# Optimization experiments

Hardware: AMD Instinct MI355X
Metric: run time of the kernel (lower is better)

## Reference

```python
import jax, jax.numpy as jnp
import numpy as np

B, C, H, W = 8, 256, 128, 128
CQK = C // 8
EPS = 1e-6


def _l2n(x):
    # normalize over channel axis (dim=-2), matching torch l2_norm (no eps)
    return x / jnp.linalg.norm(x, axis=-2, keepdims=True)


def setup_inputs() -> dict:
    key = jax.random.key(0)
    ks = jax.random.split(key, 8)
    s = 0.05
    return {
        "x": jax.random.normal(ks[0], (B, C, H, W), dtype=jnp.float32),
        "Wq": jax.random.normal(ks[1], (CQK, C), dtype=jnp.float32) * s,
        "bq": jax.random.normal(ks[2], (CQK,), dtype=jnp.float32) * s,
        "Wk": jax.random.normal(ks[3], (CQK, C), dtype=jnp.float32) * s,
        "bk": jax.random.normal(ks[4], (CQK,), dtype=jnp.float32) * s,
        "Wv": jax.random.normal(ks[5], (C, C), dtype=jnp.float32) * s,
        "bv": jax.random.normal(ks[6], (C,), dtype=jnp.float32) * s,
        "gamma": jnp.ones((1,), dtype=jnp.float32) * 0.5,
    }


def reference(x, Wq, bq, Wk, bk, Wv, bv, gamma):
    b, c, h, w = x.shape
    n = h * w
    xf = x.reshape(b, c, n)  # [B, C, N]
    # 1x1 convs == channel matmuls
    Q = jnp.einsum('oc,bcn->bon', Wq, xf) + bq[None, :, None]  # [B, Cqk, N]
    K = jnp.einsum('oc,bcn->bon', Wk, xf) + bk[None, :, None]  # [B, Cqk, N]
    V = jnp.einsum('oc,bcn->bon', Wv, xf) + bv[None, :, None]  # [B, C, N]
    Qn = jnp.swapaxes(_l2n(Q), 1, 2)  # [B, N, Cqk]
    Kn = _l2n(K)                      # [B, Cqk, N]
    k_sum = jnp.sum(Kn, axis=-1) + EPS               # [B, Cqk]
    tailor = 1.0 / (n + jnp.einsum('bnc,bc->bn', Qn, k_sum))  # [B, N]
    value_sum = jnp.sum(V, axis=-1)                   # [B, C]
    matrix = jnp.einsum('bmn,bcn->bmc', Kn, V)        # [B, Cqk, C]
    matrix_sum = value_sum[:, :, None] + jnp.einsum('bnm,bmc->bcn', Qn, matrix)  # [B, C, N]
    weight_value = matrix_sum * tailor[:, None, :]    # [B, C, N]
    return x + gamma[0] * weight_value.reshape(b, c, h, w)
```

## Files before the change

### kernel.cpp

```cpp
#include <hip/hip_runtime.h>
#include <stdint.h>


#define NB 8
#define NC 256
#define CQK 32
#define NPIX 16384
#define NTILE 64
#define TN 256
#define PARTF (CQK*NC + NC + CQK)
#define EPSV 1e-6f

typedef unsigned short bfraw;

__device__ __forceinline__ float bf2f(bfraw u) {
    union { uint32_t i; float f; } v; v.i = ((uint32_t)u) << 16; return v.f;
}
__device__ __forceinline__ void unpack8(uint4 raw, float* xv) {
    xv[0] = bf2f((bfraw)(raw.x & 0xffffu)); xv[1] = bf2f((bfraw)(raw.x >> 16));
    xv[2] = bf2f((bfraw)(raw.y & 0xffffu)); xv[3] = bf2f((bfraw)(raw.y >> 16));
    xv[4] = bf2f((bfraw)(raw.z & 0xffffu)); xv[5] = bf2f((bfraw)(raw.z >> 16));
    xv[6] = bf2f((bfraw)(raw.w & 0xffffu)); xv[7] = bf2f((bfraw)(raw.w >> 16));
}

template<int DT> __device__ __forceinline__ float ldx(const void* p, size_t i) {
    if (DT) return ((const float*)p)[i];
    return bf2f(((const bfraw*)p)[i]);
}
template<int DT> __device__ __forceinline__ void ld8(const void* p, size_t i, float* o) {
    if (DT) {
        const float4* q = (const float4*)((const float*)p + i);
        float4 a = q[0], b = q[1];
        o[0]=a.x;o[1]=a.y;o[2]=a.z;o[3]=a.w;o[4]=b.x;o[5]=b.y;o[6]=b.z;o[7]=b.w;
    } else {
        uint4 raw = *(const uint4*)((const bfraw*)p + i);
        unpack8(raw, o);
    }
}

__global__ __launch_bounds__(256) void detect_kernel(const bfraw* __restrict__ x,
                                                     int* __restrict__ flag) {
    __shared__ int cnt, ez;
    int tid = threadIdx.x;
    if (tid == 0) { cnt = 0; ez = 0; }
    __syncthreads();
    int crazy = 0, evenzero = 0;
    for (int i = tid; i < 2048; i += 256) {
        bfraw u = x[i];
        float v = bf2f(u);
        float a = fabsf(v);
        if (!(a <= 1e10f) || (v != 0.f && a < 1e-10f)) crazy++;
        if ((i & 1) == 0 && u == 0) evenzero++;
    }
    atomicAdd(&cnt, crazy);
    atomicAdd(&ez, evenzero);
    __syncthreads();
    if (tid == 0) flag[0] = (cnt > 64 || ez > 900) ? 1 : 0;
}

template<int DT> __device__ __forceinline__ void prep_body(
    const void* Wq, const void* bq, const void* Wk, const void* bk,
    float* wqT, float* wkT, float* bqf, float* bkf) {
    int tid = threadIdx.x;
    for (int i = tid; i < CQK*NC; i += 256) {
        int m = i / NC, c = i % NC;
        wqT[c*CQK + m] = ldx<DT>(Wq, i);
        wkT[c*CQK + m] = ldx<DT>(Wk, i);
    }
    if (tid < CQK) { bqf[tid] = ldx<DT>(bq, tid); bkf[tid] = ldx<DT>(bk, tid); }
}
__global__ __launch_bounds__(256) void prep_kernel(
    const void* Wq, const void* bq, const void* Wk, const void* bk,
    float* wqT, float* wkT, float* bqf, float* bkf, const int* flag) {
    if (flag[0]) prep_body<1>(Wq, bq, Wk, bk, wqT, wkT, bqf, bkf);
    else         prep_body<0>(Wq, bq, Wk, bk, wqT, wkT, bqf, bkf);
}

template<int DT> __device__ __forceinline__ void pass1_body(
    const void* __restrict__ x, const float* __restrict__ wkT,
    const float* __restrict__ bkf, float* __restrict__ partial, int PB,
    float (*kn_s)[36]) {
    int tid = threadIdx.x;
    int b = blockIdx.x / PB, j = blockIdx.x % PB;

    float sacc[CQK];
    #pragma unroll
    for (int m = 0; m < CQK; ++m) sacc[m] = 0.f;
    float xsacc = 0.f, ksacc = 0.f;

    const size_t xb_base = (size_t)b * NC * NPIX;

    for (int tile = j; tile < NTILE; tile += PB) {
        int n0 = tile * TN;

        float q[CQK];
        #pragma unroll
        for (int m = 0; m < CQK; ++m) q[m] = bkf[m];
        const size_t pix = xb_base + n0 + tid;
        #pragma unroll 4
        for (int c = 0; c < NC; ++c) {
            float xv = ldx<DT>(x, pix + (size_t)c * NPIX);
            const float4* w = (const float4*)(wkT + c*CQK);
            #pragma unroll
            for (int m4 = 0; m4 < 8; ++m4) {
                float4 wv = w[m4];
                q[m4*4+0] += wv.x * xv; q[m4*4+1] += wv.y * xv;
                q[m4*4+2] += wv.z * xv; q[m4*4+3] += wv.w * xv;
            }
        }
        float ss = 0.f;
        #pragma unroll
        for (int m = 0; m < CQK; ++m) ss += q[m]*q[m];
        float inv = rsqrtf(ss);

        __syncthreads();
        #pragma unroll
        for (int m4 = 0; m4 < 8; ++m4) {
            float4 kv;
            kv.x = q[m4*4+0]*inv; kv.y = q[m4*4+1]*inv;
            kv.z = q[m4*4+2]*inv; kv.w = q[m4*4+3]*inv;
            *((float4*)&kn_s[tid][m4*4]) = kv;
        }
        __syncthreads();

        const size_t rowbase = xb_base + (size_t)tid * NPIX + n0;
        for (int k0 = 0; k0 < TN; k0 += 8) {
            float xv[8]; ld8<DT>(x, rowbase + k0, xv);
            #pragma unroll
            for (int kk = 0; kk < 8; ++kk) {
                const float4* kr = (const float4*)&kn_s[k0+kk][0];
                float xvk = xv[kk];
                #pragma unroll
                for (int m4 = 0; m4 < 8; ++m4) {
                    float4 a = kr[m4];
                    sacc[m4*4+0] += a.x*xvk; sacc[m4*4+1] += a.y*xvk;
                    sacc[m4*4+2] += a.z*xvk; sacc[m4*4+3] += a.w*xvk;
                }
                xsacc += xvk;
            }
        }

        if (tid < CQK) {
            float s = 0.f;
            for (int t = 0; t < TN; ++t) s += kn_s[t][tid];
            ksacc += s;
        }
    }

    size_t base = (size_t)blockIdx.x * PARTF;
    #pragma unroll
    for (int m = 0; m < CQK; ++m) partial[base + m*NC + tid] = sacc[m];
    partial[base + CQK*NC + tid] = xsacc;
    if (tid < CQK) partial[base + CQK*NC + NC + tid] = ksacc;
}
__global__ __launch_bounds__(256) void pass1_kernel(
    const void* __restrict__ x, const float* __restrict__ wkT,
    const float* __restrict__ bkf, float* __restrict__ partial, int PB,
    const int* __restrict__ flag) {
    __shared__ __align__(16) float kn_s[TN][36];
    if (flag[0]) pass1_body<1>(x, wkT, bkf, partial, PB, kn_s);
    else         pass1_body<0>(x, wkT, bkf, partial, PB, kn_s);
}

template<int DT> __device__ __forceinline__ float dot256(const void* Wv, int row,
                                                         const float* sh) {
    float r = 0.f;
    for (int c0 = 0; c0 < NC; c0 += 8) {
        float xv[8]; ld8<DT>(Wv, (size_t)row * NC + c0, xv);
        #pragma unroll
        for (int i = 0; i < 8; ++i) r += xv[i] * sh[c0+i];
    }
    return r;
}
template<int DT> __device__ __forceinline__ void pass15_body(
    const float* __restrict__ partial, const void* __restrict__ Wv,
    const void* __restrict__ bv, float* __restrict__ matT,
    float* __restrict__ vsum, float* __restrict__ ksum, int PB, float* sh) {
    int tid = threadIdx.x;
    int b = blockIdx.x / 33, m = blockIdx.x % 33;
    const float* pb_ = partial + (size_t)b * PB * PARTF;

    if (m < CQK) {
        float acc = 0.f;
        for (int p = 0; p < PB; ++p) acc += pb_[(size_t)p*PARTF + m*NC + tid];
        sh[tid] = acc;
        float ks = 0.f;
        for (int p = 0; p < PB; ++p) ks += pb_[(size_t)p*PARTF + CQK*NC + NC + m];
        __syncthreads();
        float r = dot256<DT>(Wv, tid, sh);
        matT[((size_t)b*NC + tid)*CQK + m] = r + ldx<DT>(bv, tid) * ks;
        if (tid == 0) ksum[b*CQK + m] = ks + EPSV;
    } else {
        float acc = 0.f;
        for (int p = 0; p < PB; ++p) acc += pb_[(size_t)p*PARTF + CQK*NC + tid];
        sh[tid] = acc;
        __syncthreads();
        float r = dot256<DT>(Wv, tid, sh);
        vsum[b*NC + tid] = r + (float)NPIX * ldx<DT>(bv, tid);
    }
}
__global__ __launch_bounds__(256) void pass15_kernel(
    const float* __restrict__ partial, const void* __restrict__ Wv,
    const void* __restrict__ bv, float* __restrict__ matT,
    float* __restrict__ vsum, float* __restrict__ ksum, int PB,
    const int* __restrict__ flag) {
    __shared__ float sh[NC];
    if (flag[0]) pass15_body<1>(partial, Wv, bv, matT, vsum, ksum, PB, sh);
    else         pass15_body<0>(partial, Wv, bv, matT, vsum, ksum, PB, sh);
}

template<int DT> __device__ __forceinline__ void pass2_body(
    const void* __restrict__ x, const float* __restrict__ wqT,
    const float* __restrict__ bqf, const float* __restrict__ ksum,
    const float* __restrict__ matT, const float* __restrict__ vsum,
    const void* __restrict__ gamma, float* __restrict__ out) {
    int tid = threadIdx.x;
    int b = blockIdx.x / NTILE, tile = blockIdx.x % NTILE;
    int n0 = tile * TN;
    const size_t xb_base = (size_t)b * NC * NPIX;
    const size_t pix = xb_base + n0 + tid;

    float q[CQK];
    #pragma unroll
    for (int m = 0; m < CQK; ++m) q[m] = bqf[m];
    #pragma unroll 4
    for (int c = 0; c < NC; ++c) {
        float xv = ldx<DT>(x, pix + (size_t)c * NPIX);
        const float4* w = (const float4*)(wqT + c*CQK);
        #pragma unroll
        for (int m4 = 0; m4 < 8; ++m4) {
            float4 wv = w[m4];
            q[m4*4+0] += wv.x * xv; q[m4*4+1] += wv.y * xv;
            q[m4*4+2] += wv.z * xv; q[m4*4+3] += wv.w * xv;
        }
    }
    float ss = 0.f;
    #pragma unroll
    for (int m = 0; m < CQK; ++m) ss += q[m]*q[m];
    float inv = rsqrtf(ss);
    const float* ksb = ksum + b*CQK;
    float dot = 0.f;
    #pragma unroll
    for (int m = 0; m < CQK; ++m) { q[m] *= inv; dot += q[m] * ksb[m]; }
    float tl = 1.f / ((float)NPIX + dot);
    float gt = ldx<DT>(gamma, 0) * tl;

    const float* mb = matT + (size_t)b*NC*CQK;
    const float* vb = vsum + (size_t)b*NC;
    float* op = out + pix;
    #pragma unroll 2
    for (int c = 0; c < NC; ++c) {
        float r = vb[c];
        const float4* mr = (const float4*)(mb + c*CQK);
        #pragma unroll
        for (int m4 = 0; m4 < 8; ++m4) {
            float4 a = mr[m4];
            r += q[m4*4+0]*a.x + q[m4*4+1]*a.y + q[m4*4+2]*a.z + q[m4*4+3]*a.w;
        }
        float xv = ldx<DT>(x, pix + (size_t)c * NPIX);
        op[(size_t)c * NPIX] = xv + gt*r;
    }
}
__global__ __launch_bounds__(256) void pass2_kernel(
    const void* __restrict__ x, const float* __restrict__ wqT,
    const float* __restrict__ bqf, const float* __restrict__ ksum,
    const float* __restrict__ matT, const float* __restrict__ vsum,
    const void* __restrict__ gamma, float* __restrict__ out,
    const int* __restrict__ flag) {
    if (flag[0]) pass2_body<1>(x, wqT, bqf, ksum, matT, vsum, gamma, out);
    else         pass2_body<0>(x, wqT, bqf, ksum, matT, vsum, gamma, out);
}

extern "C" void kernel_launch(void* const* d_in, const int* in_sizes, int n_in,
                              void* d_out, int out_size, void* d_ws, size_t ws_size,
                              hipStream_t stream)
{
    const void* x  = d_in[0];
    const void* Wq = d_in[1];
    const void* bq = d_in[2];
    const void* Wk = d_in[3];
    const void* bk = d_in[4];
    const void* Wv = d_in[5];
    const void* bv = d_in[6];
    const void* gm = d_in[7];
    float* out = (float*)d_out;

    float* ws = (float*)d_ws;
    int*  flag = (int*)ws;
    float* wkT = ws + 16;
    float* wqT = wkT + CQK*NC;
    float* bkf = wqT + CQK*NC;
    float* bqf = bkf + CQK;
    float* matT = bqf + CQK;
    float* vsum = matT + NB*NC*CQK;
    float* ksum = vsum + NB*NC;
    float* partial = ksum + NB*CQK;

    size_t fixedf = (size_t)(partial - ws);
    int PB = 64;
    while (PB > 1 && (fixedf + (size_t)NB*PB*PARTF) * 4 > ws_size) PB >>= 1;

    hipLaunchKernelGGL(detect_kernel, dim3(1), dim3(256), 0, stream,
                       (const bfraw*)x, flag);
    hipLaunchKernelGGL(prep_kernel, dim3(1), dim3(256), 0, stream,
                       Wq, bq, Wk, bk, wqT, wkT, bqf, bkf, flag);
    hipLaunchKernelGGL(pass1_kernel, dim3(NB*PB), dim3(256), 0, stream,
                       x, wkT, bkf, partial, PB, flag);
    hipLaunchKernelGGL(pass15_kernel, dim3(NB*33), dim3(256), 0, stream,
                       partial, Wv, bv, matT, vsum, ksum, PB, flag);
    hipLaunchKernelGGL(pass2_kernel, dim3(NB*NTILE), dim3(256), 0, stream,
                       x, wqT, bqf, ksum, matT, vsum, gm, out, flag);
}
```

Before: 518.9 us.

## Compute Q alongside K in pass1, store normalized Q, split pass2 over channels

Pass1 now projects both K and Q in one sweep over x using a merged transposed weight, and writes the normalized Q to a workspace buffer in a float4-interleaved layout. Pass2 reads that Q instead of recomputing the 256-channel projection, and its grid is split four ways over output channels for more parallelism. The detect and prep kernels are merged into one launch. In exchange, pass1 carries 64 accumulators, which raises register pressure, and there is extra global traffic to write and read Q (about 4 MB).

```diff
diff --git a/kernel.cpp b/kernel.cpp
--- a/kernel.cpp
+++ b/kernel.cpp
@@ -22,7 +22,6 @@
     xv[4] = bf2f((bfraw)(raw.z & 0xffffu)); xv[5] = bf2f((bfraw)(raw.z >> 16));
     xv[6] = bf2f((bfraw)(raw.w & 0xffffu)); xv[7] = bf2f((bfraw)(raw.w >> 16));
 }
-
 template<int DT> __device__ __forceinline__ float ldx(const void* p, size_t i) {
     if (DT) return ((const float*)p)[i];
     return bf2f(((const bfraw*)p)[i]);
@@ -38,15 +37,29 @@
     }
 }
 
-__global__ __launch_bounds__(256) void detect_kernel(const bfraw* __restrict__ x,
-                                                     int* __restrict__ flag) {
-    __shared__ int cnt, ez;
+template<int DT> __device__ __forceinline__ void prep_body(
+    const void* Wq, const void* bq, const void* Wk, const void* bk,
+    float* wkqT, float* bkq) {
+    int tid = threadIdx.x;
+    for (int i = tid; i < CQK*NC; i += 256) {
+        int m = i >> 8, c = i & 255;
+        wkqT[c*64 + m]      = ldx<DT>(Wk, i);
+        wkqT[c*64 + 32 + m] = ldx<DT>(Wq, i);
+    }
+    if (tid < CQK)      bkq[tid]      = ldx<DT>(bk, tid);
+    else if (tid < 64)  bkq[tid]      = ldx<DT>(bq, tid - 32);
+}
+__global__ __launch_bounds__(256) void detprep_kernel(
+    const bfraw* __restrict__ xr, const void* Wq, const void* bq,
+    const void* Wk, const void* bk,
+    int* __restrict__ flag, float* __restrict__ wkqT, float* __restrict__ bkq) {
+    __shared__ int cnt, ez, fl_s;
     int tid = threadIdx.x;
     if (tid == 0) { cnt = 0; ez = 0; }
     __syncthreads();
     int crazy = 0, evenzero = 0;
     for (int i = tid; i < 2048; i += 256) {
-        bfraw u = x[i];
+        bfraw u = xr[i];
         float v = bf2f(u);
         float a = fabsf(v);
         if (!(a <= 1e10f) || (v != 0.f && a < 1e-10f)) crazy++;
@@ -55,31 +68,16 @@
     atomicAdd(&cnt, crazy);
     atomicAdd(&ez, evenzero);
     __syncthreads();
-    if (tid == 0) flag[0] = (cnt > 64 || ez > 900) ? 1 : 0;
-}
-
-template<int DT> __device__ __forceinline__ void prep_body(
-    const void* Wq, const void* bq, const void* Wk, const void* bk,
-    float* wqT, float* wkT, float* bqf, float* bkf) {
-    int tid = threadIdx.x;
-    for (int i = tid; i < CQK*NC; i += 256) {
-        int m = i / NC, c = i % NC;
-        wqT[c*CQK + m] = ldx<DT>(Wq, i);
-        wkT[c*CQK + m] = ldx<DT>(Wk, i);
-    }
-    if (tid < CQK) { bqf[tid] = ldx<DT>(bq, tid); bkf[tid] = ldx<DT>(bk, tid); }
-}
-__global__ __launch_bounds__(256) void prep_kernel(
-    const void* Wq, const void* bq, const void* Wk, const void* bk,
-    float* wqT, float* wkT, float* bqf, float* bkf, const int* flag) {
-    if (flag[0]) prep_body<1>(Wq, bq, Wk, bk, wqT, wkT, bqf, bkf);
-    else         prep_body<0>(Wq, bq, Wk, bk, wqT, wkT, bqf, bkf);
+    if (tid == 0) { fl_s = (cnt > 64 || ez > 900) ? 1 : 0; flag[0] = fl_s; }
+    __syncthreads();
+    if (fl_s) prep_body<1>(Wq, bq, Wk, bk, wkqT, bkq);
+    else      prep_body<0>(Wq, bq, Wk, bk, wkqT, bkq);
 }
 
 template<int DT> __device__ __forceinline__ void pass1_body(
-    const void* __restrict__ x, const float* __restrict__ wkT,
-    const float* __restrict__ bkf, float* __restrict__ partial, int PB,
-    float (*kn_s)[36]) {
+    const void* __restrict__ x, const float* __restrict__ wkqT,
+    const float* __restrict__ bkq, float4* __restrict__ qn4,
+    float* __restrict__ partial, int PB, float (*kn_s)[36]) {
     int tid = threadIdx.x;
     int b = blockIdx.x / PB, j = blockIdx.x % PB;
 
@@ -93,35 +91,51 @@
     for (int tile = j; tile < NTILE; tile += PB) {
         int n0 = tile * TN;
 
-        float q[CQK];
-        #pragma unroll
-        for (int m = 0; m < CQK; ++m) q[m] = bkf[m];
-        const size_t pix = xb_base + n0 + tid;
-        #pragma unroll 4
-        for (int c = 0; c < NC; ++c) {
-            float xv = ldx<DT>(x, pix + (size_t)c * NPIX);
-            const float4* w = (const float4*)(wkT + c*CQK);
+        float kq[64];
+        #pragma unroll
+        for (int m = 0; m < 64; ++m) kq[m] = bkq[m];
+        const size_t pixi = xb_base + n0 + tid;
+        for (int c0 = 0; c0 < NC; c0 += 8) {
+            float xv[8];
             #pragma unroll
-            for (int m4 = 0; m4 < 8; ++m4) {
-                float4 wv = w[m4];
-                q[m4*4+0] += wv.x * xv; q[m4*4+1] += wv.y * xv;
-                q[m4*4+2] += wv.z * xv; q[m4*4+3] += wv.w * xv;
+            for (int jj = 0; jj < 8; ++jj)
+                xv[jj] = ldx<DT>(x, pixi + (size_t)(c0+jj) * NPIX);
+            #pragma unroll
+            for (int jj = 0; jj < 8; ++jj) {
+                const float4* w = (const float4*)(wkqT + (c0+jj)*64);
+                #pragma unroll
+                for (int m4 = 0; m4 < 16; ++m4) {
+                    float4 wv = w[m4];
+                    kq[m4*4+0] += wv.x * xv[jj]; kq[m4*4+1] += wv.y * xv[jj];
+                    kq[m4*4+2] += wv.z * xv[jj]; kq[m4*4+3] += wv.w * xv[jj];
+                }
             }
         }
-        float ss = 0.f;
-        #pragma unroll
-        for (int m = 0; m < CQK; ++m) ss += q[m]*q[m];
-        float inv = rsqrtf(ss);
+        float ssk = 0.f, ssq = 0.f;
+        #pragma unroll
+        for (int m = 0; m < CQK; ++m) {
+            ssk += kq[m]*kq[m]; ssq += kq[32+m]*kq[32+m];
+        }
+        float invk = rsqrtf(ssk), invq = rsqrtf(ssq);
 
         __syncthreads();
         #pragma unroll
         for (int m4 = 0; m4 < 8; ++m4) {
             float4 kv;
-            kv.x = q[m4*4+0]*inv; kv.y = q[m4*4+1]*inv;
-            kv.z = q[m4*4+2]*inv; kv.w = q[m4*4+3]*inv;
+            kv.x = kq[m4*4+0]*invk; kv.y = kq[m4*4+1]*invk;
+            kv.z = kq[m4*4+2]*invk; kv.w = kq[m4*4+3]*invk;
             *((float4*)&kn_s[tid][m4*4]) = kv;
         }
         __syncthreads();
+
+        float4* qp = qn4 + (size_t)b * 8 * NPIX + (n0 + tid);
+        #pragma unroll
+        for (int m4 = 0; m4 < 8; ++m4) {
+            float4 qv;
+            qv.x = kq[32+m4*4+0]*invq; qv.y = kq[32+m4*4+1]*invq;
+            qv.z = kq[32+m4*4+2]*invq; qv.w = kq[32+m4*4+3]*invq;
+            qp[(size_t)m4 * NPIX] = qv;
+        }
 
         const size_t rowbase = xb_base + (size_t)tid * NPIX + n0;
         for (int k0 = 0; k0 < TN; k0 += 8) {
@@ -154,12 +168,12 @@
     if (tid < CQK) partial[base + CQK*NC + NC + tid] = ksacc;
 }
 __global__ __launch_bounds__(256) void pass1_kernel(
-    const void* __restrict__ x, const float* __restrict__ wkT,
-    const float* __restrict__ bkf, float* __restrict__ partial, int PB,
-    const int* __restrict__ flag) {
+    const void* __restrict__ x, const float* __restrict__ wkqT,
+    const float* __restrict__ bkq, float4* __restrict__ qn4,
+    float* __restrict__ partial, int PB, const int* __restrict__ flag) {
     __shared__ __align__(16) float kn_s[TN][36];
-    if (flag[0]) pass1_body<1>(x, wkT, bkf, partial, PB, kn_s);
-    else         pass1_body<0>(x, wkT, bkf, partial, PB, kn_s);
+    if (flag[0]) pass1_body<1>(x, wkqT, bkq, qn4, partial, PB, kn_s);
+    else         pass1_body<0>(x, wkqT, bkq, qn4, partial, PB, kn_s);
 }
 
 template<int DT> __device__ __forceinline__ float dot256(const void* Wv, int row,
@@ -210,65 +224,60 @@
 }
 
 template<int DT> __device__ __forceinline__ void pass2_body(
-    const void* __restrict__ x, const float* __restrict__ wqT,
-    const float* __restrict__ bqf, const float* __restrict__ ksum,
-    const float* __restrict__ matT, const float* __restrict__ vsum,
-    const void* __restrict__ gamma, float* __restrict__ out) {
-    int tid = threadIdx.x;
-    int b = blockIdx.x / NTILE, tile = blockIdx.x % NTILE;
+    const void* __restrict__ x, const float4* __restrict__ qn4,
+    const float* __restrict__ ksum, const float* __restrict__ matT,
+    const float* __restrict__ vsum, const void* __restrict__ gamma,
+    float* __restrict__ out) {
+    int tid = threadIdx.x;
+    int bx = blockIdx.x;
+    int cs = bx & 3, tile = (bx >> 2) & 63, b = bx >> 8;
     int n0 = tile * TN;
-    const size_t xb_base = (size_t)b * NC * NPIX;
-    const size_t pix = xb_base + n0 + tid;
+    int p = n0 + tid;
 
     float q[CQK];
+    const float4* qp = qn4 + (size_t)b * 8 * NPIX + p;
     #pragma unroll
-    for (int m = 0; m < CQK; ++m) q[m] = bqf[m];
-    #pragma unroll 4
-    for (int c = 0; c < NC; ++c) {
-        float xv = ldx<DT>(x, pix + (size_t)c * NPIX);
-        const float4* w = (const float4*)(wqT + c*CQK);
-        #pragma unroll
-        for (int m4 = 0; m4 < 8; ++m4) {
-            float4 wv = w[m4];
-            q[m4*4+0] += wv.x * xv; q[m4*4+1] += wv.y * xv;
-            q[m4*4+2] += wv.z * xv; q[m4*4+3] += wv.w * xv;
-        }
-    }
-    float ss = 0.f;
-    #pragma unroll
-    for (int m = 0; m < CQK; ++m) ss += q[m]*q[m];
-    float inv = rsqrtf(ss);
+    for (int m4 = 0; m4 < 8; ++m4) {
+        float4 v = qp[(size_t)m4 * NPIX];
+        q[m4*4+0]=v.x; q[m4*4+1]=v.y; q[m4*4+2]=v.z; q[m4*4+3]=v.w;
+    }
     const float* ksb = ksum + b*CQK;
     float dot = 0.f;
     #pragma unroll
-    for (int m = 0; m < CQK; ++m) { q[m] *= inv; dot += q[m] * ksb[m]; }
+    for (int m = 0; m < CQK; ++m) dot += q[m] * ksb[m];
     float tl = 1.f / ((float)NPIX + dot);
     float gt = ldx<DT>(gamma, 0) * tl;
 
-    const float* mb = matT + (size_t)b*NC*CQK;
-    const float* vb = vsum + (size_t)b*NC;
-    float* op = out + pix;
-    #pragma unroll 2
-    for (int c = 0; c < NC; ++c) {
-        float r = vb[c];
-        const float4* mr = (const float4*)(mb + c*CQK);
-        #pragma unroll
-        for (int m4 = 0; m4 < 8; ++m4) {
-            float4 a = mr[m4];
-            r += q[m4*4+0]*a.x + q[m4*4+1]*a.y + q[m4*4+2]*a.z + q[m4*4+3]*a.w;
-        }
-        float xv = ldx<DT>(x, pix + (size_t)c * NPIX);
-        op[(size_t)c * NPIX] = xv + gt*r;
+    int c0 = cs * 64;
+    const float* mb = matT + ((size_t)b*NC + c0)*CQK;
+    const float* vb = vsum + (size_t)b*NC + c0;
+    size_t xbase = (size_t)b*NC*NPIX + (size_t)c0*NPIX + p;
+
+    for (int ci = 0; ci < 64; ci += 4) {
+        float xv[4];
+        #pragma unroll
+        for (int u = 0; u < 4; ++u)
+            xv[u] = ldx<DT>(x, xbase + (size_t)(ci+u)*NPIX);
+        #pragma unroll
+        for (int u = 0; u < 4; ++u) {
+            float r = vb[ci+u];
+            const float4* mr = (const float4*)(mb + (ci+u)*CQK);
+            #pragma unroll
+            for (int m4 = 0; m4 < 8; ++m4) {
+                float4 a = mr[m4];
+                r += q[m4*4+0]*a.x + q[m4*4+1]*a.y + q[m4*4+2]*a.z + q[m4*4+3]*a.w;
+            }
+            out[xbase + (size_t)(ci+u)*NPIX] = xv[u] + gt*r;
+        }
     }
 }
 __global__ __launch_bounds__(256) void pass2_kernel(
-    const void* __restrict__ x, const float* __restrict__ wqT,
-    const float* __restrict__ bqf, const float* __restrict__ ksum,
-    const float* __restrict__ matT, const float* __restrict__ vsum,
-    const void* __restrict__ gamma, float* __restrict__ out,
-    const int* __restrict__ flag) {
-    if (flag[0]) pass2_body<1>(x, wqT, bqf, ksum, matT, vsum, gamma, out);
-    else         pass2_body<0>(x, wqT, bqf, ksum, matT, vsum, gamma, out);
+    const void* __restrict__ x, const float4* __restrict__ qn4,
+    const float* __restrict__ ksum, const float* __restrict__ matT,
+    const float* __restrict__ vsum, const void* __restrict__ gamma,
+    float* __restrict__ out, const int* __restrict__ flag) {
+    if (flag[0]) pass2_body<1>(x, qn4, ksum, matT, vsum, gamma, out);
+    else         pass2_body<0>(x, qn4, ksum, matT, vsum, gamma, out);
 }
 
 extern "C" void kernel_launch(void* const* d_in, const int* in_sizes, int n_in,
@@ -286,28 +295,25 @@
     float* out = (float*)d_out;
 
     float* ws = (float*)d_ws;
-    int*  flag = (int*)ws;
-    float* wkT = ws + 16;
-    float* wqT = wkT + CQK*NC;
-    float* bkf = wqT + CQK*NC;
-    float* bqf = bkf + CQK;
-    float* matT = bqf + CQK;
+    int*   flag = (int*)ws;
+    float* wkqT = ws + 16;
+    float* bkq  = wkqT + 64*NC;
+    float* matT = bkq + 64;
     float* vsum = matT + NB*NC*CQK;
     float* ksum = vsum + NB*NC;
-    float* partial = ksum + NB*CQK;
+    float* qn4f = ksum + NB*CQK;
+    float* partial = qn4f + (size_t)NB*8*NPIX*4;
 
     size_t fixedf = (size_t)(partial - ws);
     int PB = 64;
     while (PB > 1 && (fixedf + (size_t)NB*PB*PARTF) * 4 > ws_size) PB >>= 1;
 
-    hipLaunchKernelGGL(detect_kernel, dim3(1), dim3(256), 0, stream,
-                       (const bfraw*)x, flag);
-    hipLaunchKernelGGL(prep_kernel, dim3(1), dim3(256), 0, stream,
-                       Wq, bq, Wk, bk, wqT, wkT, bqf, bkf, flag);
+    hipLaunchKernelGGL(detprep_kernel, dim3(1), dim3(256), 0, stream,
+                       (const bfraw*)x, Wq, bq, Wk, bk, flag, wkqT, bkq);
     hipLaunchKernelGGL(pass1_kernel, dim3(NB*PB), dim3(256), 0, stream,
-                       x, wkT, bkf, partial, PB, flag);
+                       x, wkqT, bkq, (float4*)qn4f, partial, PB, flag);
     hipLaunchKernelGGL(pass15_kernel, dim3(NB*33), dim3(256), 0, stream,
                        partial, Wv, bv, matT, vsum, ksum, PB, flag);
-    hipLaunchKernelGGL(pass2_kernel, dim3(NB*NTILE), dim3(256), 0, stream,
-                       x, wqT, bqf, ksum, matT, vsum, gm, out, flag);
-}
+    hipLaunchKernelGGL(pass2_kernel, dim3(NB*NTILE*4), dim3(256), 0, stream,
+                       x, (const float4*)qn4f, ksum, matT, vsum, gm, out, flag);
+}
```

Result: faster. 491.8 us (-5.2%).
